# Performance work log

Measured on AMD Instinct MI355X. Metric: run time of the kernel, lower is better.

## Reference

```python
import jax, jax.numpy as jnp
import numpy as np

B, N, E, L = 64, 50000, 1600000, 20
BN_EPS = 1e-5


def setup_inputs() -> dict:
    key = jax.random.key(0)
    ks = jax.random.split(key, 8)
    x = jax.random.normal(ks[0], (B, N), dtype=jnp.float32)
    edge_index = jax.random.randint(ks[1], (2, E), 0, N, dtype=jnp.int32)
    alpha = jax.random.normal(ks[2], (E,), dtype=jnp.float32)
    bias = jax.random.normal(ks[3], (E,), dtype=jnp.float32)
    # LazyLinear(num_labels) on [B, N] features
    W = jax.random.normal(ks[4], (L, N), dtype=jnp.float32) / np.sqrt(N)
    b_lin = jax.random.normal(ks[5], (L,), dtype=jnp.float32) * 0.01
    # LazyBatchNorm1d affine params over N features
    gamma = jnp.ones((N,), dtype=jnp.float32)
    beta = jnp.zeros((N,), dtype=jnp.float32)
    return {"x": x, "edge_index": edge_index, "alpha": alpha, "bias": bias,
            "W": W, "b_lin": b_lin, "gamma": gamma, "beta": beta}


def reference(x, edge_index, alpha, bias, W, b_lin, gamma, beta):
    src, dst = edge_index[0], edge_index[1]
    # gather per-edge source features and apply per-edge affine: [B, E]
    x_e = alpha * x[:, src] + bias
    # scatter-mean into destination nodes: [B, N]
    sums = jnp.zeros((x.shape[0], N), dtype=x.dtype).at[:, dst].add(x_e)
    counts = jnp.zeros((N,), dtype=x.dtype).at[dst].add(1.0)
    x_hat = sums / jnp.maximum(counts, 1.0)
    out = jnp.tanh(x_hat)
    # linear head: [B, L]
    pred = x_hat @ W.T + b_lin
    # BatchNorm1d (training mode: batch stats, biased variance)
    mu = jnp.mean(out, axis=0)
    var = jnp.var(out, axis=0)
    bn = (out - mu) / jnp.sqrt(var + BN_EPS) * gamma + beta
    return (pred, bn)
```

## Files before the change

### kernel.cpp

```cpp
#include <hip/hip_runtime.h>
#include <math.h>

#define NB 64
#define NL 20
#define BN_EPS 1e-5f

#define BIN_W 32
#define NBIN 1563
#define BIN_CAP 1280
#define CHUNK 4096

#define NSB 49
#define NSBP 64
#define CAP1 36864
#define NSLICE 9

__device__ __forceinline__ unsigned short f2bf(float f) {
    unsigned u = __float_as_uint(f);
    unsigned r = u + 0x7fff + ((u >> 16) & 1);
    return (unsigned short)(r >> 16);
}
__device__ __forceinline__ float bf2f(unsigned short h) {
    return __uint_as_float(((unsigned)h) << 16);
}

__global__ __launch_bounds__(256) void transpose_kernel(
    const float* __restrict__ x, unsigned short* __restrict__ xTb, int Nn) {
    __shared__ float tile[64][65];
    int n0 = blockIdx.x * 64;
    int ln = threadIdx.x & 63;
    int wv = threadIdx.x >> 6;
    for (int r = wv; r < 64; r += 4) {
        int col = n0 + ln;
        tile[r][ln] = (col < Nn) ? x[r * Nn + col] : 0.f;
    }
    __syncthreads();
    for (int r = wv; r < 64; r += 4) {
        int node = n0 + r;
        if (node < Nn) xTb[(size_t)node * 64 + ln] = f2bf(tile[ln][r]);
    }
}

__global__ __launch_bounds__(1024) void binA_kernel(
    const int* __restrict__ src, const int* __restrict__ dst,
    const float* __restrict__ alpha, const float* __restrict__ bias,
    int* __restrict__ cnt1, uint2* __restrict__ buf1, int E) {
    __shared__ unsigned hist[NSBP];
    __shared__ unsigned gbase[NSBP];

    int tid = threadIdx.x;
    int e0 = blockIdx.x * CHUNK;

    if (tid < NSBP) hist[tid] = 0;
    __syncthreads();

    uint2 pay[4];
    unsigned rk[4];
    int sb[4];
    #pragma unroll
    for (int k = 0; k < 4; ++k) {
        int e = e0 + k * 1024 + tid;
        sb[k] = -1;
        if (e < E) {
            int d = dst[e];
            int b = d >> 5;
            int dl = d & 31;
            pay[k].x = (unsigned)src[e] | ((unsigned)f2bf(alpha[e]) << 16);
            pay[k].y = (unsigned)f2bf(bias[e]) | ((unsigned)dl << 16) |
                       ((unsigned)b << 21);
            sb[k] = d >> 10;
            rk[k] = atomicAdd(&hist[sb[k]], 1u);
        }
    }
    __syncthreads();

    if (tid < NSBP) {
        unsigned v = hist[tid];
        if (v > 0) gbase[tid] = (unsigned)atomicAdd(&cnt1[tid], (int)v);
    }
    __syncthreads();

    #pragma unroll
    for (int k = 0; k < 4; ++k) {
        if (sb[k] >= 0) {
            unsigned di = gbase[sb[k]] + rk[k];
            if (di < CAP1)
                buf1[(size_t)sb[k] * CAP1 + di] = pay[k];
        }
    }
}

__global__ __launch_bounds__(1024) void binB_kernel(
    const int* __restrict__ cnt1, const uint2* __restrict__ buf1,
    int* __restrict__ cursor, uint2* __restrict__ paybins) {
    __shared__ unsigned hist[32];
    __shared__ unsigned gbase[32];

    int tid = threadIdx.x;
    int sb = blockIdx.x / NSLICE;
    int slice = blockIdx.x % NSLICE;

    int lim = cnt1[sb];
    if (lim > CAP1) lim = CAP1;
    int cc = lim - slice * 4096;
    if (cc < 0) cc = 0;
    if (cc > 4096) cc = 4096;
    const uint2* pb = buf1 + (size_t)sb * CAP1 + (size_t)slice * 4096;

    if (tid < 32) hist[tid] = 0;
    __syncthreads();

    uint2 pay[4];
    unsigned rk[4];
    int lb[4];
    #pragma unroll
    for (int k = 0; k < 4; ++k) {
        int i = k * 1024 + tid;
        lb[k] = -1;
        if (i < cc) {
            pay[k] = pb[i];
            lb[k] = (int)((pay[k].y >> 21) & 31u);
            rk[k] = atomicAdd(&hist[lb[k]], 1u);
        }
    }
    __syncthreads();

    if (tid < 32) {
        unsigned v = hist[tid];
        if (v > 0)
            gbase[tid] = (unsigned)atomicAdd(&cursor[sb * 32 + tid], (int)v);
    }
    __syncthreads();

    #pragma unroll
    for (int k = 0; k < 4; ++k) {
        if (lb[k] >= 0) {
            int bin = sb * 32 + lb[k];
            unsigned di = gbase[lb[k]] + rk[k];
            if (di < BIN_CAP)
                paybins[(size_t)bin * BIN_CAP + di] = pay[k];
        }
    }
}

__global__ __launch_bounds__(256) void pull_fin3_kernel(
    const int* __restrict__ cursor, const uint2* __restrict__ paybins,
    const unsigned short* __restrict__ xTb, const float* __restrict__ W,
    const float* __restrict__ gamma, const float* __restrict__ beta,
    float* __restrict__ pred_part, float* __restrict__ bn, int Nn) {
    __shared__ __align__(16) char smem[16640];
    uint2* ed = (uint2*)smem;
    float (*xh)[65] = (float (*)[65])smem;
    float (*th)[65] = (float (*)[65])(smem + 8320);

    __shared__ float wl[NL][32];
    __shared__ unsigned h2[32], b2[32], c2[32];
    __shared__ float mu_s[32], a_s[32], be_s[32];

    int bin = blockIdx.x;
    int tid = threadIdx.x;
    int ln = tid & 63;
    int w = tid >> 6;
    int n0 = bin * 32;

    int cnt = cursor[bin];
    if (cnt > BIN_CAP) cnt = BIN_CAP;
    const uint2* pb = paybins + (size_t)bin * BIN_CAP;

    for (int i = tid; i < NL * 32; i += 256) {
        int l = i >> 5, j = i & 31;
        wl[l][j] = (n0 + j < Nn) ? W[l * Nn + n0 + j] : 0.f;
    }
    if (tid < 32) { h2[tid] = 0; c2[tid] = 0; }
    __syncthreads();

    uint2 pA = {0, 0}, pB = {0, 0}, pC = {0, 0}, pD = {0, 0}, pE = {0, 0};
    {
        int i;
        i = tid;
        if (i < cnt) { pA = pb[i]; atomicAdd(&h2[(pA.y >> 16) & 31], 1u); }
        i = tid + 256;
        if (i < cnt) { pB = pb[i]; atomicAdd(&h2[(pB.y >> 16) & 31], 1u); }
        i = tid + 512;
        if (i < cnt) { pC = pb[i]; atomicAdd(&h2[(pC.y >> 16) & 31], 1u); }
        i = tid + 768;
        if (i < cnt) { pD = pb[i]; atomicAdd(&h2[(pD.y >> 16) & 31], 1u); }
        i = tid + 1024;
        if (i < cnt) { pE = pb[i]; atomicAdd(&h2[(pE.y >> 16) & 31], 1u); }
    }
    __syncthreads();

    if (tid < 32) {
        unsigned v = h2[tid];
        unsigned incl = v;
        #pragma unroll
        for (int off = 1; off < 32; off <<= 1) {
            unsigned t = __shfl_up(incl, off, 64);
            if (tid >= off) incl += t;
        }
        b2[tid] = incl - v;
    }
    __syncthreads();

    {
        if (tid < cnt) {
            unsigned dl = (pA.y >> 16) & 31;
            ed[b2[dl] + atomicAdd(&c2[dl], 1u)] = pA;
        }
        if (tid + 256 < cnt) {
            unsigned dl = (pB.y >> 16) & 31;
            ed[b2[dl] + atomicAdd(&c2[dl], 1u)] = pB;
        }
        if (tid + 512 < cnt) {
            unsigned dl = (pC.y >> 16) & 31;
            ed[b2[dl] + atomicAdd(&c2[dl], 1u)] = pC;
        }
        if (tid + 768 < cnt) {
            unsigned dl = (pD.y >> 16) & 31;
            ed[b2[dl] + atomicAdd(&c2[dl], 1u)] = pD;
        }
        if (tid + 1024 < cnt) {
            unsigned dl = (pE.y >> 16) & 31;
            ed[b2[dl] + atomicAdd(&c2[dl], 1u)] = pE;
        }
    }
    __syncthreads();

    float xh_reg[8], th_reg[8];
    #pragma unroll
    for (int k = 0; k < 8; ++k) {
        int dl = w * 8 + k;
        int node = n0 + dl;
        int n = (int)h2[dl];
        unsigned bs = b2[dl];
        float a0 = 0.f, a1 = 0.f, a2 = 0.f, a3 = 0.f, bsum = 0.f;
        int j = 0;
        for (; j + 3 < n; j += 4) {
            uint2 e0 = ed[bs + j];
            uint2 e1 = ed[bs + j + 1];
            uint2 e2 = ed[bs + j + 2];
            uint2 e3 = ed[bs + j + 3];
            bsum += __uint_as_float((e0.y & 0xffffu) << 16) +
                    __uint_as_float((e1.y & 0xffffu) << 16) +
                    __uint_as_float((e2.y & 0xffffu) << 16) +
                    __uint_as_float((e3.y & 0xffffu) << 16);
            a0 = fmaf(__uint_as_float(e0.x & 0xffff0000u),
                      bf2f(xTb[(size_t)(e0.x & 0xffffu) * 64 + ln]), a0);
            a1 = fmaf(__uint_as_float(e1.x & 0xffff0000u),
                      bf2f(xTb[(size_t)(e1.x & 0xffffu) * 64 + ln]), a1);
            a2 = fmaf(__uint_as_float(e2.x & 0xffff0000u),
                      bf2f(xTb[(size_t)(e2.x & 0xffffu) * 64 + ln]), a2);
            a3 = fmaf(__uint_as_float(e3.x & 0xffff0000u),
                      bf2f(xTb[(size_t)(e3.x & 0xffffu) * 64 + ln]), a3);
        }
        for (; j < n; ++j) {
            uint2 e0 = ed[bs + j];
            bsum += __uint_as_float((e0.y & 0xffffu) << 16);
            a0 = fmaf(__uint_as_float(e0.x & 0xffff0000u),
                      bf2f(xTb[(size_t)(e0.x & 0xffffu) * 64 + ln]), a0);
        }
        float xhat = 0.f;
        if (node < Nn)
            xhat = ((a0 + a1) + (a2 + a3) + bsum) / fmaxf((float)n, 1.0f);
        xh_reg[k] = xhat;
        float tv = tanhf(xhat);
        th_reg[k] = tv;

        float s = tv, q = tv * tv;
        #pragma unroll
        for (int off = 32; off > 0; off >>= 1) {
            s += __shfl_xor(s, off, 64);
            q += __shfl_xor(q, off, 64);
        }
        if (ln == 0) {
            float mu = s * (1.0f / 64.0f);
            float var = fmaxf(q * (1.0f / 64.0f) - mu * mu, 0.f);
            float inv = rsqrtf(var + BN_EPS);
            float gm = 1.f, bt = 0.f;
            if (node < Nn) { gm = gamma[node]; bt = beta[node]; }
            mu_s[dl] = mu;
            a_s[dl] = inv * gm;
            be_s[dl] = bt;
        }
    }
    __syncthreads();

    #pragma unroll
    for (int k = 0; k < 8; ++k) {
        xh[w * 8 + k][ln] = xh_reg[k];
        th[w * 8 + k][ln] = th_reg[k];
    }
    __syncthreads();

    {
        float acc[5] = {0.f, 0.f, 0.f, 0.f, 0.f};
        for (int n = 0; n < 32; ++n) {
            float xv = xh[n][ln];
            #pragma unroll
            for (int k = 0; k < 5; ++k)
                acc[k] = fmaf(xv, wl[w + k * 4][n], acc[k]);
        }
        #pragma unroll
        for (int k = 0; k < 5; ++k)
            pred_part[(size_t)bin * (NB * NL) + ln * NL + (w + k * 4)] = acc[k];
    }

    for (int idx = tid; idx < 32 * 64; idx += 256) {
        int noff = idx & 31, bb = idx >> 5;
        int node = n0 + noff;
        if (node < Nn)
            bn[bb * Nn + node] =
                fmaf(th[noff][bb] - mu_s[noff], a_s[noff], be_s[noff]);
    }
}

__global__ __launch_bounds__(256) void reduce_pred_kernel(
    const float* __restrict__ part, const float* __restrict__ b_lin,
    float* __restrict__ pred, int nblk) {
    int out = blockIdx.x * 4 + (threadIdx.x >> 6);
    if (out >= NB * NL) return;
    int ln = threadIdx.x & 63;
    float s = 0.f;
    for (int i = ln; i < nblk; i += 64)
        s += part[(size_t)i * (NB * NL) + out];
    #pragma unroll
    for (int off = 32; off > 0; off >>= 1)
        s += __shfl_xor(s, off, 64);
    if (ln == 0) pred[out] = b_lin[out % NL] + s;
}

extern "C" void kernel_launch(void* const* d_in, const int* in_sizes, int n_in,
                              void* d_out, int out_size, void* d_ws, size_t ws_size,
                              hipStream_t stream) {
    const float* x     = (const float*)d_in[0];
    const int*   ei    = (const int*)d_in[1];
    const float* alpha = (const float*)d_in[2];
    const float* bias  = (const float*)d_in[3];
    const float* W     = (const float*)d_in[4];
    const float* b_lin = (const float*)d_in[5];
    const float* gamma = (const float*)d_in[6];
    const float* beta  = (const float*)d_in[7];

    const int Nn = in_sizes[0] / NB;
    const int E  = in_sizes[1] / 2;
    const int* src = ei;
    const int* dst = ei + E;

    const int ntile = (Nn + 63) / 64;

    uint2*          paybins = (uint2*)d_ws;
    uint2*          buf1    = paybins + (size_t)NBIN * BIN_CAP;
    float*          pred_part = (float*)buf1;
    unsigned short* xTb     = (unsigned short*)(buf1 + (size_t)NSB * CAP1);
    int*            cnt1    = (int*)(xTb + (size_t)Nn * 64);
    int*            cursor  = cnt1 + NSBP;

    float* pred = (float*)d_out;
    float* bn   = pred + NB * NL;

    hipMemsetAsync(cnt1, 0, (NSBP + NBIN + 32) * sizeof(int), stream);

    transpose_kernel<<<ntile, 256, 0, stream>>>(x, xTb, Nn);
    binA_kernel<<<(E + CHUNK - 1) / CHUNK, 1024, 0, stream>>>(
        src, dst, alpha, bias, cnt1, buf1, E);
    binB_kernel<<<NSB * NSLICE, 1024, 0, stream>>>(cnt1, buf1, cursor, paybins);
    pull_fin3_kernel<<<NBIN, 256, 0, stream>>>(cursor, paybins, xTb, W,
                                               gamma, beta, pred_part, bn, Nn);
    reduce_pred_kernel<<<(NB * NL + 3) / 4, 256, 0, stream>>>(
        pred_part, b_lin, pred, NBIN);
}
```

Measured before the change: 197.8 us.

## Fuse transpose into binning kernel and gather bf16 pairs per lane in pull

Merges the transpose and first binning pass into one launch, with block ranges split by role, so independent work shares a single grid and one launch is removed. In the pull kernel, each lane now loads a 32-bit word holding two bf16 batch values. Each half-wave handles a different edge, and the halves are combined with a cross-lane shuffle. This halves the number of gather instructions per edge. The cost is a strided shared-memory store layout with padding changed to 66, plus extra shuffles.

New measurement: 188.9 us. 4.5% less time.

```diff
diff --git a/kernel.cpp b/kernel.cpp
--- a/kernel.cpp
+++ b/kernel.cpp
@@ -20,72 +20,69 @@
     unsigned r = u + 0x7fff + ((u >> 16) & 1);
     return (unsigned short)(r >> 16);
 }
-__device__ __forceinline__ float bf2f(unsigned short h) {
-    return __uint_as_float(((unsigned)h) << 16);
-}
-
-__global__ __launch_bounds__(256) void transpose_kernel(
-    const float* __restrict__ x, unsigned short* __restrict__ xTb, int Nn) {
-    __shared__ float tile[64][65];
-    int n0 = blockIdx.x * 64;
-    int ln = threadIdx.x & 63;
-    int wv = threadIdx.x >> 6;
-    for (int r = wv; r < 64; r += 4) {
-        int col = n0 + ln;
-        tile[r][ln] = (col < Nn) ? x[r * Nn + col] : 0.f;
-    }
-    __syncthreads();
-    for (int r = wv; r < 64; r += 4) {
-        int node = n0 + r;
-        if (node < Nn) xTb[(size_t)node * 64 + ln] = f2bf(tile[ln][r]);
-    }
-}
-
-__global__ __launch_bounds__(1024) void binA_kernel(
+
+__global__ __launch_bounds__(1024) void stage_kernel(
+    const float* __restrict__ x, unsigned short* __restrict__ xTb,
     const int* __restrict__ src, const int* __restrict__ dst,
     const float* __restrict__ alpha, const float* __restrict__ bias,
-    int* __restrict__ cnt1, uint2* __restrict__ buf1, int E) {
+    int* __restrict__ cnt1, uint2* __restrict__ buf1, int E, int Nn, int nA) {
     __shared__ unsigned hist[NSBP];
     __shared__ unsigned gbase[NSBP];
+    __shared__ float tile[64][65];
 
     int tid = threadIdx.x;
-    int e0 = blockIdx.x * CHUNK;
-
-    if (tid < NSBP) hist[tid] = 0;
-    __syncthreads();
-
-    uint2 pay[4];
-    unsigned rk[4];
-    int sb[4];
-    #pragma unroll
-    for (int k = 0; k < 4; ++k) {
-        int e = e0 + k * 1024 + tid;
-        sb[k] = -1;
-        if (e < E) {
-            int d = dst[e];
-            int b = d >> 5;
-            int dl = d & 31;
-            pay[k].x = (unsigned)src[e] | ((unsigned)f2bf(alpha[e]) << 16);
-            pay[k].y = (unsigned)f2bf(bias[e]) | ((unsigned)dl << 16) |
-                       ((unsigned)b << 21);
-            sb[k] = d >> 10;
-            rk[k] = atomicAdd(&hist[sb[k]], 1u);
-        }
-    }
-    __syncthreads();
-
-    if (tid < NSBP) {
-        unsigned v = hist[tid];
-        if (v > 0) gbase[tid] = (unsigned)atomicAdd(&cnt1[tid], (int)v);
-    }
-    __syncthreads();
-
-    #pragma unroll
-    for (int k = 0; k < 4; ++k) {
-        if (sb[k] >= 0) {
-            unsigned di = gbase[sb[k]] + rk[k];
-            if (di < CAP1)
-                buf1[(size_t)sb[k] * CAP1 + di] = pay[k];
+
+    if ((int)blockIdx.x < nA) {
+        int e0 = blockIdx.x * CHUNK;
+        if (tid < NSBP) hist[tid] = 0;
+        __syncthreads();
+
+        uint2 pay[4];
+        unsigned rk[4];
+        int sb[4];
+        #pragma unroll
+        for (int k = 0; k < 4; ++k) {
+            int e = e0 + k * 1024 + tid;
+            sb[k] = -1;
+            if (e < E) {
+                int d = dst[e];
+                int b = d >> 5;
+                int dl = d & 31;
+                pay[k].x = (unsigned)src[e] | ((unsigned)f2bf(alpha[e]) << 16);
+                pay[k].y = (unsigned)f2bf(bias[e]) | ((unsigned)dl << 16) |
+                           ((unsigned)b << 21);
+                sb[k] = d >> 10;
+                rk[k] = atomicAdd(&hist[sb[k]], 1u);
+            }
+        }
+        __syncthreads();
+
+        if (tid < NSBP) {
+            unsigned v = hist[tid];
+            if (v > 0) gbase[tid] = (unsigned)atomicAdd(&cnt1[tid], (int)v);
+        }
+        __syncthreads();
+
+        #pragma unroll
+        for (int k = 0; k < 4; ++k) {
+            if (sb[k] >= 0) {
+                unsigned di = gbase[sb[k]] + rk[k];
+                if (di < CAP1)
+                    buf1[(size_t)sb[k] * CAP1 + di] = pay[k];
+            }
+        }
+    } else {
+        int n0 = ((int)blockIdx.x - nA) * 64;
+        int ln = tid & 63;
+        int wv = tid >> 6;
+        for (int r = wv; r < 64; r += 16) {
+            int col = n0 + ln;
+            tile[r][ln] = (col < Nn) ? x[r * Nn + col] : 0.f;
+        }
+        __syncthreads();
+        for (int r = wv; r < 64; r += 16) {
+            int node = n0 + r;
+            if (node < Nn) xTb[(size_t)node * 64 + ln] = f2bf(tile[ln][r]);
         }
     }
 }
@@ -143,25 +140,29 @@
     }
 }
 
-__global__ __launch_bounds__(256) void pull_fin3_kernel(
+__global__ __launch_bounds__(256) void pull_fin4_kernel(
     const int* __restrict__ cursor, const uint2* __restrict__ paybins,
     const unsigned short* __restrict__ xTb, const float* __restrict__ W,
     const float* __restrict__ gamma, const float* __restrict__ beta,
     float* __restrict__ pred_part, float* __restrict__ bn, int Nn) {
-    __shared__ __align__(16) char smem[16640];
+    __shared__ __align__(16) char smem[16896];
     uint2* ed = (uint2*)smem;
-    float (*xh)[65] = (float (*)[65])smem;
-    float (*th)[65] = (float (*)[65])(smem + 8320);
+    float (*xh)[66] = (float (*)[66])smem;
+    float (*th)[66] = (float (*)[66])(smem + 8448);
 
     __shared__ float wl[NL][32];
     __shared__ unsigned h2[32], b2[32], c2[32];
     __shared__ float mu_s[32], a_s[32], be_s[32];
+
+    const unsigned* xTbu = (const unsigned*)xTb;
 
     int bin = blockIdx.x;
     int tid = threadIdx.x;
     int ln = tid & 63;
     int w = tid >> 6;
     int n0 = bin * 32;
+    int pair = ln >> 5;
+    int h = ln & 31;
 
     int cnt = cursor[bin];
     if (cnt > BIN_CAP) cnt = BIN_CAP;
@@ -226,45 +227,54 @@
     }
     __syncthreads();
 
-    float xh_reg[8], th_reg[8];
+    float xv_reg[8], tv_reg[8];
     #pragma unroll
     for (int k = 0; k < 8; ++k) {
         int dl = w * 8 + k;
         int node = n0 + dl;
         int n = (int)h2[dl];
         unsigned bs = b2[dl];
-        float a0 = 0.f, a1 = 0.f, a2 = 0.f, a3 = 0.f, bsum = 0.f;
+        float accL0 = 0.f, accH0 = 0.f, accL1 = 0.f, accH1 = 0.f;
+        float bs0 = 0.f, bs1 = 0.f;
         int j = 0;
         for (; j + 3 < n; j += 4) {
-            uint2 e0 = ed[bs + j];
-            uint2 e1 = ed[bs + j + 1];
-            uint2 e2 = ed[bs + j + 2];
-            uint2 e3 = ed[bs + j + 3];
-            bsum += __uint_as_float((e0.y & 0xffffu) << 16) +
-                    __uint_as_float((e1.y & 0xffffu) << 16) +
-                    __uint_as_float((e2.y & 0xffffu) << 16) +
-                    __uint_as_float((e3.y & 0xffffu) << 16);
-            a0 = fmaf(__uint_as_float(e0.x & 0xffff0000u),
-                      bf2f(xTb[(size_t)(e0.x & 0xffffu) * 64 + ln]), a0);
-            a1 = fmaf(__uint_as_float(e1.x & 0xffff0000u),
-                      bf2f(xTb[(size_t)(e1.x & 0xffffu) * 64 + ln]), a1);
-            a2 = fmaf(__uint_as_float(e2.x & 0xffff0000u),
-                      bf2f(xTb[(size_t)(e2.x & 0xffffu) * 64 + ln]), a2);
-            a3 = fmaf(__uint_as_float(e3.x & 0xffff0000u),
-                      bf2f(xTb[(size_t)(e3.x & 0xffffu) * 64 + ln]), a3);
-        }
-        for (; j < n; ++j) {
-            uint2 e0 = ed[bs + j];
-            bsum += __uint_as_float((e0.y & 0xffffu) << 16);
-            a0 = fmaf(__uint_as_float(e0.x & 0xffff0000u),
-                      bf2f(xTb[(size_t)(e0.x & 0xffffu) * 64 + ln]), a0);
-        }
-        float xhat = 0.f;
-        if (node < Nn)
-            xhat = ((a0 + a1) + (a2 + a3) + bsum) / fmaxf((float)n, 1.0f);
-        xh_reg[k] = xhat;
-        float tv = tanhf(xhat);
-        th_reg[k] = tv;
+            uint2 e0 = ed[bs + j + pair];
+            uint2 e1 = ed[bs + j + 2 + pair];
+            unsigned v0 = xTbu[(size_t)(e0.x & 0xffffu) * 32 + h];
+            unsigned v1 = xTbu[(size_t)(e1.x & 0xffffu) * 32 + h];
+            float al0 = __uint_as_float(e0.x & 0xffff0000u);
+            float al1 = __uint_as_float(e1.x & 0xffff0000u);
+            bs0 += __uint_as_float((e0.y & 0xffffu) << 16);
+            bs1 += __uint_as_float((e1.y & 0xffffu) << 16);
+            accL0 = fmaf(al0, __uint_as_float(v0 << 16), accL0);
+            accH0 = fmaf(al0, __uint_as_float(v0 & 0xffff0000u), accH0);
+            accL1 = fmaf(al1, __uint_as_float(v1 << 16), accL1);
+            accH1 = fmaf(al1, __uint_as_float(v1 & 0xffff0000u), accH1);
+        }
+        for (; j < n; j += 2) {
+            int idx = j + pair;
+            bool act = idx < n;
+            uint2 e0 = ed[act ? (bs + idx) : bs];
+            float al0 = act ? __uint_as_float(e0.x & 0xffff0000u) : 0.f;
+            float bi0 = act ? __uint_as_float((e0.y & 0xffffu) << 16) : 0.f;
+            unsigned v0 = xTbu[(size_t)(e0.x & 0xffffu) * 32 + h];
+            bs0 += bi0;
+            accL0 = fmaf(al0, __uint_as_float(v0 << 16), accL0);
+            accH0 = fmaf(al0, __uint_as_float(v0 & 0xffff0000u), accH0);
+        }
+        float accL = accL0 + accL1;
+        float accH = accH0 + accH1;
+        float bsum = bs0 + bs1;
+        accL += __shfl_xor(accL, 32, 64);
+        accH += __shfl_xor(accH, 32, 64);
+        bsum += __shfl_xor(bsum, 32, 64);
+        float inv = 1.0f / fmaxf((float)n, 1.0f);
+        float xlo = (accL + bsum) * inv;
+        float xhi = (accH + bsum) * inv;
+        float xv = pair ? xhi : xlo;
+        float tv = tanhf(xv);
+        xv_reg[k] = xv;
+        tv_reg[k] = tv;
 
         float s = tv, q = tv * tv;
         #pragma unroll
@@ -275,20 +285,23 @@
         if (ln == 0) {
             float mu = s * (1.0f / 64.0f);
             float var = fmaxf(q * (1.0f / 64.0f) - mu * mu, 0.f);
-            float inv = rsqrtf(var + BN_EPS);
+            float invs = rsqrtf(var + BN_EPS);
             float gm = 1.f, bt = 0.f;
             if (node < Nn) { gm = gamma[node]; bt = beta[node]; }
             mu_s[dl] = mu;
-            a_s[dl] = inv * gm;
+            a_s[dl] = invs * gm;
             be_s[dl] = bt;
         }
     }
     __syncthreads();
 
-    #pragma unroll
-    for (int k = 0; k < 8; ++k) {
-        xh[w * 8 + k][ln] = xh_reg[k];
-        th[w * 8 + k][ln] = th_reg[k];
+    {
+        int col = 2 * h + pair;
+        #pragma unroll
+        for (int k = 0; k < 8; ++k) {
+            xh[w * 8 + k][col] = xv_reg[k];
+            th[w * 8 + k][col] = tv_reg[k];
+        }
     }
     __syncthreads();
 
@@ -347,6 +360,7 @@
     const int* dst = ei + E;
 
     const int ntile = (Nn + 63) / 64;
+    const int nA    = (E + CHUNK - 1) / CHUNK;
 
     uint2*          paybins = (uint2*)d_ws;
     uint2*          buf1    = paybins + (size_t)NBIN * BIN_CAP;
@@ -360,11 +374,10 @@
 
     hipMemsetAsync(cnt1, 0, (NSBP + NBIN + 32) * sizeof(int), stream);
 
-    transpose_kernel<<<ntile, 256, 0, stream>>>(x, xTb, Nn);
-    binA_kernel<<<(E + CHUNK - 1) / CHUNK, 1024, 0, stream>>>(
-        src, dst, alpha, bias, cnt1, buf1, E);
+    stage_kernel<<<nA + ntile, 1024, 0, stream>>>(
+        x, xTb, src, dst, alpha, bias, cnt1, buf1, E, Nn, nA);
     binB_kernel<<<NSB * NSLICE, 1024, 0, stream>>>(cnt1, buf1, cursor, paybins);
-    pull_fin3_kernel<<<NBIN, 256, 0, stream>>>(cursor, paybins, xTb, W,
+    pull_fin4_kernel<<<NBIN, 256, 0, stream>>>(cursor, paybins, xTb, W,
                                                gamma, beta, pred_part, bn, Nn);
     reduce_pred_kernel<<<(NB * NL + 3) / 4, 256, 0, stream>>>(
         pred_part, b_lin, pred, NBIN);
```
